# Kernel tuning notes

Measured on AMD Instinct MI355X. Metric: run time of the kernel, lower is better.

## Reference

```python
import jax, jax.numpy as jnp
import numpy as np

NEG = -1000000.0  # same finite mask value as the Triton kernel


def setup_inputs() -> dict:
    key = jax.random.key(0)
    k1, k2, k3, k4 = jax.random.split(key, 4)
    B, H, KVH, S, D = 1, 32, 8, 2048, 128
    return {
        "q": jax.random.normal(k1, (B, H, S, D), dtype=jnp.float32),
        "k": jax.random.normal(k2, (B, KVH, S, D), dtype=jnp.float32),
        "v": jax.random.normal(k3, (B, KVH, S, D), dtype=jnp.float32),
        "sinks": jax.random.normal(k4, (H,), dtype=jnp.float32),
        "bandwidth": 1024,
    }


def reference(q, k, v, sinks, bandwidth):
    """Prefill flash attention with causal + sliding-window masking, GQA, and
    per-head attention sinks (extra logit in the softmax denominator)."""
    B, H, S, D = q.shape
    ratio = H // k.shape[1]  # KV_HEAD_RATIO
    kf = jnp.repeat(k, ratio, axis=1)  # [B,H,S,D]
    vf = jnp.repeat(v, ratio, axis=1)
    sm_scale = 1.0 / np.sqrt(D).astype(np.float32)

    logits = jnp.einsum("bhqd,bhkd->bhqk", q, kf) * sm_scale  # [B,H,S,S]
    q_pos = jnp.arange(S)[:, None]
    k_pos = jnp.arange(S)[None, :]
    mask = k_pos > q_pos  # causal
    if bandwidth > 0:
        mask = mask | (k_pos < q_pos - bandwidth + 1)  # sliding window
    logits = jnp.where(mask, NEG, logits)

    sink = sinks[None, :, None]  # [1,H,1] broadcast over batch, query
    m = jnp.maximum(jnp.max(logits, axis=-1), sink)  # [B,H,S]
    p = jnp.exp(logits - m[..., None])
    denom = p.sum(axis=-1) + jnp.exp(sink - m)  # sink contributes to denom only
    out = jnp.einsum("bhqk,bhkd->bhqd", p, vf) / denom[..., None]
    return out
```

## Files before the change

kernel.cpp:

```cpp
#include <hip/hip_runtime.h>
#include <hip/hip_bf16.h>

typedef __bf16 bf16x8 __attribute__((ext_vector_type(8)));
typedef unsigned short u16x8 __attribute__((ext_vector_type(8)));
typedef unsigned int u32x4 __attribute__((ext_vector_type(4)));
typedef float f32x4 __attribute__((ext_vector_type(4)));

#define SLEN 2048
#define DDIM 128
#define NH   32
#define NKVH 8
#define KVB  32
#define MINIT  -1e30f
#define MASKED -3e30f
#define LOG2E  1.4426950408889634f

static __device__ __forceinline__ unsigned short f2bfu(float f) {
  union { float f; unsigned u; } x; x.f = f;
  return (unsigned short)((x.u + 0x7fffu + ((x.u >> 16) & 1u)) >> 16);
}
static __device__ __forceinline__ float bfu2f(unsigned short u) {
  union { unsigned u; float f; } x; x.u = ((unsigned)u) << 16;
  return x.f;
}
static __device__ __forceinline__ unsigned cvt_pk_bf16(float lo, float hi) {
  unsigned r;
  asm("v_cvt_pk_bf16_f32 %0, %1, %2" : "=v"(r) : "v"(lo), "v"(hi));
  return r;
}
static __device__ __forceinline__ f32x4 mfma_bf16(u16x8 a, u16x8 b, f32x4 c) {
  return __builtin_amdgcn_mfma_f32_16x16x32_bf16(
      __builtin_bit_cast(bf16x8, a), __builtin_bit_cast(bf16x8, b), c, 0, 0, 0);
}
static __device__ __forceinline__ int vswz_k(int row) {
  return (row & 3) | (((row >> 3) & 1) << 2);
}

__global__ __launch_bounds__(256) void conv_kv(const float* __restrict__ k,
                                               const float* __restrict__ v,
                                               unsigned* __restrict__ kdst,
                                               unsigned short* __restrict__ vt) {
  __shared__ unsigned T32[32][17];
  const int bb = blockIdx.x;
  if (bb < 1024) {
    const int i = bb * 256 + threadIdx.x;
    const float4 f0 = ((const float4*)k)[2 * i];
    const float4 f1 = ((const float4*)k)[2 * i + 1];
    u32x4 o = { cvt_pk_bf16(f0.x, f0.y), cvt_pk_bf16(f0.z, f0.w),
                cvt_pk_bf16(f1.x, f1.y), cvt_pk_bf16(f1.z, f1.w) };
    ((u32x4*)kdst)[i] = o;
    return;
  }
  const int b   = bb - 1024;
  const int dt  = b & 3;
  const int st  = (b >> 2) & 63;
  const int kvh = b >> 8;
  const int r  = threadIdx.x >> 3;
  const int cg = threadIdx.x & 7;
  const float4 f = *(const float4*)(v + ((size_t)(kvh * SLEN + st * 32 + r) * DDIM) + dt * 32 + cg * 4);
  T32[r][cg * 2]     = cvt_pk_bf16(f.x, f.y);
  T32[r][cg * 2 + 1] = cvt_pk_bf16(f.z, f.w);
  __syncthreads();
  const int dr = threadIdx.x >> 3;
  const unsigned sel = (dr & 1) ? 0x07060302u : 0x05040100u;
  const unsigned a0 = T32[cg * 4 + 0][dr >> 1], a1 = T32[cg * 4 + 1][dr >> 1];
  const unsigned a2 = T32[cg * 4 + 2][dr >> 1], a3 = T32[cg * 4 + 3][dr >> 1];
  unsigned short* vp = vt + (size_t)kvh * DDIM * SLEN + (size_t)(dt * 32 + dr) * SLEN + st * 32 + cg * 4;
  const unsigned w0 = __builtin_amdgcn_perm(a1, a0, sel);
  const unsigned w1 = __builtin_amdgcn_perm(a3, a2, sel);
  vp[0] = (unsigned short)(w0 & 0xffff);
  vp[1] = (unsigned short)(w0 >> 16);
  vp[2] = (unsigned short)(w1 & 0xffff);
  vp[3] = (unsigned short)(w1 >> 16);
}

template <int NCH>
__global__ __launch_bounds__(256, 4) void attn_fwd(
    const float* __restrict__ q, const unsigned short* __restrict__ kbf,
    const unsigned short* __restrict__ vtg, const float* __restrict__ sinks,
    const int* __restrict__ bwp, float* __restrict__ out,
    unsigned short* __restrict__ pO, float* __restrict__ pm,
    float* __restrict__ pl) {
  constexpr int NQT = 32;
  __shared__ unsigned short Kl[2][KVB * DDIM];
  __shared__ unsigned short Vt[2][DDIM * KVB];
  __shared__ float SmS[4][16];

  const int tid  = threadIdx.x;
  const int wid  = tid >> 6;
  const int lane = tid & 63;
  const int ln   = lane & 15;
  const int hi   = lane >> 4;

  const int B   = blockIdx.x;
  const int x   = B & 7;
  const int j   = B >> 3;
  constexpr int per = 4 * NCH;
  const int qt  = NQT - 1 - (j / per);
  const int rem = j % per;
  const int hh  = rem / NCH;
  const int c   = rem % NCH;
  const int h   = x * 4 + hh;
  const int kvh = x;
  const int q0  = qt * 64;
  const int qrow0 = q0 + wid * 16;
  const int qpos  = qrow0 + ln;

  const int bwv    = bwp[0];
  const int lo_off = (bwv > 0) ? (bwv - 1) : SLEN;

  const int T0 = max(0, q0 - lo_off) >> 5;
  const int T1 = (q0 + 63) >> 5;
  const int N  = T1 - T0 + 1;
  const int ch = (N + NCH - 1) / NCH;
  const int Ts = T0 + c * ch;
  const int Te = min(T1, Ts + ch - 1);

  const float c2 = 0.08838834764831845f * LOG2E;

  u16x8 qf[4];
  {
    const float* qp = q + ((size_t)(h * SLEN + qpos) * DDIM) + hi * 8;
    #pragma unroll
    for (int dk = 0; dk < 4; ++dk) {
      float4 f0 = *(const float4*)(qp + dk * 32);
      float4 f1 = *(const float4*)(qp + dk * 32 + 4);
      u32x4 t = { cvt_pk_bf16(f0.x, f0.y), cvt_pk_bf16(f0.z, f0.w),
                  cvt_pk_bf16(f1.x, f1.y), cvt_pk_bf16(f1.z, f1.w) };
      qf[dk] = __builtin_bit_cast(u16x8, t);
    }
  }

  float m2 = MINIT, l_ln = 0.0f;
  f32x4 oacc[8];
  #pragma unroll
  for (int nt = 0; nt < 8; ++nt) oacc[nt] = f32x4{0.f, 0.f, 0.f, 0.f};

  const unsigned short* Kg = kbf + (size_t)kvh * SLEN * DDIM;
  const unsigned short* Vg = vtg + (size_t)kvh * DDIM * SLEN;

  const int kr0 = tid >> 4, sk = tid & 15;
  const int kr1 = kr0 + 16;
  const int kw0 = kr0 * DDIM + (((sk & 8) | ((sk & 7) ^ vswz_k(kr0))) * 8);
  const int kw1 = kr1 * DDIM + (((sk & 8) | ((sk & 7) ^ vswz_k(kr1))) * 8);
  const int vr0 = tid >> 2, sv = tid & 3;
  const int vr1 = vr0 + 64;
  const int vw0 = vr0 * KVB + ((sv ^ ((vr0 >> 1) & 3)) * 8);
  const int vw1 = vr1 * KVB + ((sv ^ ((vr1 >> 1) & 3)) * 8);

  const int prow = ((ln >> 2) << 3) | (ln & 3);
  const int vk   = (ln & 3) | (((ln >> 2) & 1) << 2);
  int kfo[4];
  #pragma unroll
  for (int dk = 0; dk < 4; ++dk) {
    const int s = dk * 4 + hi;
    kfo[dk] = prow * DDIM + (((s & 8) | ((s & 7) ^ vk)) * 8);
  }
  const int vro = ln * KVB + ((hi ^ ((ln >> 1) & 3)) * 8);

  if (Ts <= Te) {
    const int kbS = Ts * 32, kbE = Te * 32;

    u16x8 pk0, pk1, pv0, pv1;
    pk0 = *(const u16x8*)(Kg + (size_t)(kbS + kr0) * DDIM + sk * 8);
    pk1 = *(const u16x8*)(Kg + (size_t)(kbS + kr1) * DDIM + sk * 8);
    pv0 = *(const u16x8*)(Vg + (size_t)vr0 * SLEN + kbS + sv * 8);
    pv1 = *(const u16x8*)(Vg + (size_t)vr1 * SLEN + kbS + sv * 8);
    *(u16x8*)&Kl[0][kw0] = pk0;
    *(u16x8*)&Kl[0][kw1] = pk1;
    *(u16x8*)&Vt[0][vw0] = pv0;
    *(u16x8*)&Vt[0][vw1] = pv1;
    {
      const int nb = min(kbS + KVB, kbE);
      pk0 = *(const u16x8*)(Kg + (size_t)(nb + kr0) * DDIM + sk * 8);
      pk1 = *(const u16x8*)(Kg + (size_t)(nb + kr1) * DDIM + sk * 8);
      pv0 = *(const u16x8*)(Vg + (size_t)vr0 * SLEN + nb + sv * 8);
      pv1 = *(const u16x8*)(Vg + (size_t)vr1 * SLEN + nb + sv * 8);
    }

    int cur = 0;
    for (int kb = kbS; kb <= kbE; kb += KVB) {
      __syncthreads();
      const int nxt = cur ^ 1;
      *(u16x8*)&Kl[nxt][kw0] = pk0;
      *(u16x8*)&Kl[nxt][kw1] = pk1;
      *(u16x8*)&Vt[nxt][vw0] = pv0;
      *(u16x8*)&Vt[nxt][vw1] = pv1;
      {
        const int nb = min(kb + 2 * KVB, kbE);
        pk0 = *(const u16x8*)(Kg + (size_t)(nb + kr0) * DDIM + sk * 8);
        pk1 = *(const u16x8*)(Kg + (size_t)(nb + kr1) * DDIM + sk * 8);
        pv0 = *(const u16x8*)(Vg + (size_t)vr0 * SLEN + nb + sv * 8);
        pv1 = *(const u16x8*)(Vg + (size_t)vr1 * SLEN + nb + sv * 8);
      }

      const bool skip = (kb > qrow0 + 15) || (kb + KVB - 1 < qrow0 - lo_off);
      if (!skip) {
        const unsigned short* kbp = &Kl[cur][0];
        const unsigned short* vbp = &Vt[cur][0];

        f32x4 sacc0 = {0,0,0,0}, sacc1 = {0,0,0,0};
        __builtin_amdgcn_s_setprio(1);
        #pragma unroll
        for (int dk = 0; dk < 4; ++dk) {
          sacc0 = mfma_bf16(*(const u16x8*)(kbp + kfo[dk]), qf[dk], sacc0);
          sacc1 = mfma_bf16(*(const u16x8*)(kbp + kfo[dk] + 4 * DDIM), qf[dk], sacc1);
        }
        __builtin_amdgcn_s_setprio(0);

        float p[8];
        const bool interior = (kb + KVB - 1 <= qrow0) && (kb >= qrow0 + 15 - lo_off);
        if (interior) {
          #pragma unroll
          for (int r = 0; r < 4; ++r) {
            p[r]     = sacc0[r] * c2;
            p[4 + r] = sacc1[r] * c2;
          }
        } else {
          #pragma unroll
          for (int r = 0; r < 4; ++r) {
            const int kp0 = kb + hi * 8 + r;
            const int kp1 = kp0 + 4;
            p[r]     = ((kp0 <= qpos) && (kp0 >= qpos - lo_off)) ? sacc0[r] * c2 : MASKED;
            p[4 + r] = ((kp1 <= qpos) && (kp1 >= qpos - lo_off)) ? sacc1[r] * c2 : MASKED;
          }
        }

        float mx = fmaxf(fmaxf(fmaxf(p[0], p[1]), fmaxf(p[2], p[3])),
                         fmaxf(fmaxf(p[4], p[5]), fmaxf(p[6], p[7])));
        mx = fmaxf(mx, __shfl_xor(mx, 16));
        mx = fmaxf(mx, __shfl_xor(mx, 32));

        if (__any(mx > m2 + 11.5415605f)) {
          const float mn   = fmaxf(m2, mx);
          const float corr = exp2f(m2 - mn);
          l_ln *= corr;
          m2 = mn;
          if (hi == 0) SmS[wid][ln] = corr;
          float c4[4];
          #pragma unroll
          for (int r = 0; r < 4; ++r) c4[r] = SmS[wid][hi * 4 + r];
          #pragma unroll
          for (int nt = 0; nt < 8; ++nt)
            #pragma unroll
            for (int r = 0; r < 4; ++r) oacc[nt][r] *= c4[r];
        }

        float s = 0.0f;
        #pragma unroll
        for (int jj = 0; jj < 8; ++jj) { p[jj] = exp2f(p[jj] - m2); s += p[jj]; }
        s += __shfl_xor(s, 16);
        s += __shfl_xor(s, 32);
        l_ln += s;

        const u32x4 paw = { cvt_pk_bf16(p[0], p[1]), cvt_pk_bf16(p[2], p[3]),
                            cvt_pk_bf16(p[4], p[5]), cvt_pk_bf16(p[6], p[7]) };
        const u16x8 pa = __builtin_bit_cast(u16x8, paw);

        __builtin_amdgcn_s_setprio(1);
        #pragma unroll
        for (int nt = 0; nt < 8; ++nt) {
          const u16x8 vb = *(const u16x8*)(vbp + vro + nt * 16 * KVB);
          oacc[nt] = mfma_bf16(pa, vb, oacc[nt]);
        }
        __builtin_amdgcn_s_setprio(0);
      }
      cur ^= 1;
    }
  }

  if (NCH == 1) {
    const float sk2 = sinks[h] * LOG2E;
    const float M  = fmaxf(m2, sk2);
    const float ed = exp2f(m2 - M);
    const float fac_ln = ed / (l_ln * ed + exp2f(sk2 - M));
    if (hi == 0) SmS[wid][ln] = fac_ln;
    float fac4[4];
    #pragma unroll
    for (int r = 0; r < 4; ++r) fac4[r] = SmS[wid][hi * 4 + r];
    #pragma unroll
    for (int r = 0; r < 4; ++r) {
      float* op = out + ((size_t)(h * SLEN + qrow0 + hi*4 + r) * DDIM) + ln;
      #pragma unroll
      for (int nt = 0; nt < 8; ++nt) op[nt * 16] = oacc[nt][r] * fac4[r];
    }
  } else {
    const size_t Lb = ((size_t)(h * NQT + qt)) * NCH + c;
    if (hi == 0) {
      pm[Lb * 64 + wid * 16 + ln] = m2;
      pl[Lb * 64 + wid * 16 + ln] = l_ln;
    }
    #pragma unroll
    for (int r = 0; r < 4; ++r) {
      unsigned short* po = pO + (Lb * 64 + wid * 16 + hi * 4 + r) * 128 + ln;
      #pragma unroll
      for (int nt = 0; nt < 8; ++nt) po[nt * 16] = f2bfu(oacc[nt][r]);
    }
  }
}

template <int NCH, int QBLK, int NQT>
__global__ __launch_bounds__(256) void mergeN(
    const unsigned short* __restrict__ pO, const float* __restrict__ pm,
    const float* __restrict__ pl, const float* __restrict__ sinks,
    float* __restrict__ out) {
  const int t    = blockIdx.x * 256 + threadIdx.x;
  const int rid  = t >> 2;
  const int d0   = (t & 3) * 32;
  const int h    = rid >> 11;
  const int qpos = rid & 2047;
  const int qt   = qpos / QBLK;
  const int lr   = qpos % QBLK;
  const size_t base = ((size_t)(h * NQT + qt) * NCH) * QBLK + lr;
  const float sk2 = sinks[h] * LOG2E;
  float mc[NCH], lc[NCH];
  float M = sk2;
  #pragma unroll
  for (int c = 0; c < NCH; ++c) {
    mc[c] = pm[base + (size_t)c * QBLK];
    lc[c] = pl[base + (size_t)c * QBLK];
    M = fmaxf(M, mc[c]);
  }
  float denom = exp2f(sk2 - M);
  float sc[NCH];
  #pragma unroll
  for (int c = 0; c < NCH; ++c) { sc[c] = exp2f(mc[c] - M); denom += lc[c] * sc[c]; }
  const float inv = 1.0f / denom;
  float o[32];
  #pragma unroll
  for (int i = 0; i < 32; ++i) o[i] = 0.f;
  #pragma unroll
  for (int c = 0; c < NCH; ++c) {
    const unsigned short* pp = pO + (base + (size_t)c * QBLK) * 128 + d0;
    const float s = sc[c] * inv;
    #pragma unroll
    for (int i = 0; i < 4; ++i) {
      u16x8 a = *(const u16x8*)(pp + i * 8);
      #pragma unroll
      for (int jj = 0; jj < 8; ++jj) o[i*8+jj] += bfu2f(a[jj]) * s;
    }
  }
  float* op = out + (size_t)rid * 128 + d0;
  #pragma unroll
  for (int i = 0; i < 8; ++i)
    *(float4*)(op + i*4) = make_float4(o[i*4], o[i*4+1], o[i*4+2], o[i*4+3]);
}

extern "C" void kernel_launch(void* const* d_in, const int* in_sizes, int n_in,
                              void* d_out, int out_size, void* d_ws, size_t ws_size,
                              hipStream_t stream) {
  const float* q     = (const float*)d_in[0];
  const float* k     = (const float*)d_in[1];
  const float* v     = (const float*)d_in[2];
  const float* sinks = (const float*)d_in[3];
  const int*   bw    = (const int*)d_in[4];
  float* out = (float*)d_out;

  const size_t kvElems = (size_t)NKVH * SLEN * DDIM;
  unsigned short* kbf = (unsigned short*)d_ws;
  unsigned short* vtg = kbf + kvElems;
  unsigned short* pO  = vtg + kvElems;

  const size_t nPart2 = (size_t)NH * 32 * 2 * 64;
  const size_t need2  = 4 * kvElems + nPart2 * 128 * 2 + nPart2 * 8;

  conv_kv<<<dim3(1024 + NKVH * 64 * 4), 256, 0, stream>>>(k, v, (unsigned*)kbf, vtg);

  if (ws_size >= need2) {
    float* pm = (float*)(pO + nPart2 * 128);
    float* pl = pm + nPart2;
    attn_fwd<2><<<dim3(2048), 256, 0, stream>>>(q, kbf, vtg, sinks, bw, out, pO, pm, pl);
    mergeN<2, 64, 32><<<dim3(1024), 256, 0, stream>>>(pO, pm, pl, sinks, out);
  } else {
    attn_fwd<1><<<dim3(1024), 256, 0, stream>>>(q, kbf, vtg, sinks, bw, out, pO, nullptr, nullptr);
  }
}
```

Baseline: 77.75 us.

## Single-buffer K/V LDS tiles, defer row-sum shuffles, remap merge blocks by KV head

Replaces the double-buffered K/V shared-memory tiles with a single buffer guarded by two barriers per iteration, and prefetches the next tile from global memory into registers only one step ahead. This halves LDS use, which may allow more resident blocks, but it serialises the LDS store with compute and adds a barrier. The per-iteration cross-lane reduction of the row sum is moved to a single reduction after the loop. The merge kernel's block-to-row mapping is changed to group heads by KV head.

```diff
diff --git a/kernel.cpp b/kernel.cpp
--- a/kernel.cpp
+++ b/kernel.cpp
@@ -82,8 +82,8 @@
     unsigned short* __restrict__ pO, float* __restrict__ pm,
     float* __restrict__ pl) {
   constexpr int NQT = 32;
-  __shared__ unsigned short Kl[2][KVB * DDIM];
-  __shared__ unsigned short Vt[2][DDIM * KVB];
+  __shared__ unsigned short Kl[KVB * DDIM];
+  __shared__ unsigned short Vt[DDIM * KVB];
   __shared__ float SmS[4][16];
 
   const int tid  = threadIdx.x;
@@ -131,7 +131,8 @@
     }
   }
 
-  float m2 = MINIT, l_ln = 0.0f;
+  float m2 = MINIT;
+  float l_ln = 0.0f;
   f32x4 oacc[8];
   #pragma unroll
   for (int nt = 0; nt < 8; ++nt) oacc[nt] = f32x4{0.f, 0.f, 0.f, 0.f};
@@ -162,112 +163,100 @@
     const int kbS = Ts * 32, kbE = Te * 32;
 
     u16x8 pk0, pk1, pv0, pv1;
-    pk0 = *(const u16x8*)(Kg + (size_t)(kbS + kr0) * DDIM + sk * 8);
-    pk1 = *(const u16x8*)(Kg + (size_t)(kbS + kr1) * DDIM + sk * 8);
-    pv0 = *(const u16x8*)(Vg + (size_t)vr0 * SLEN + kbS + sv * 8);
-    pv1 = *(const u16x8*)(Vg + (size_t)vr1 * SLEN + kbS + sv * 8);
-    *(u16x8*)&Kl[0][kw0] = pk0;
-    *(u16x8*)&Kl[0][kw1] = pk1;
-    *(u16x8*)&Vt[0][vw0] = pv0;
-    *(u16x8*)&Vt[0][vw1] = pv1;
     {
-      const int nb = min(kbS + KVB, kbE);
-      pk0 = *(const u16x8*)(Kg + (size_t)(nb + kr0) * DDIM + sk * 8);
-      pk1 = *(const u16x8*)(Kg + (size_t)(nb + kr1) * DDIM + sk * 8);
-      pv0 = *(const u16x8*)(Vg + (size_t)vr0 * SLEN + nb + sv * 8);
-      pv1 = *(const u16x8*)(Vg + (size_t)vr1 * SLEN + nb + sv * 8);
-    }
-
-    int cur = 0;
+      pk0 = *(const u16x8*)(Kg + (size_t)(kbS + kr0) * DDIM + sk * 8);
+      pk1 = *(const u16x8*)(Kg + (size_t)(kbS + kr1) * DDIM + sk * 8);
+      pv0 = *(const u16x8*)(Vg + (size_t)vr0 * SLEN + kbS + sv * 8);
+      pv1 = *(const u16x8*)(Vg + (size_t)vr1 * SLEN + kbS + sv * 8);
+    }
+
     for (int kb = kbS; kb <= kbE; kb += KVB) {
       __syncthreads();
-      const int nxt = cur ^ 1;
-      *(u16x8*)&Kl[nxt][kw0] = pk0;
-      *(u16x8*)&Kl[nxt][kw1] = pk1;
-      *(u16x8*)&Vt[nxt][vw0] = pv0;
-      *(u16x8*)&Vt[nxt][vw1] = pv1;
+      *(u16x8*)&Kl[kw0] = pk0;
+      *(u16x8*)&Kl[kw1] = pk1;
+      *(u16x8*)&Vt[vw0] = pv0;
+      *(u16x8*)&Vt[vw1] = pv1;
+      __syncthreads();
+
       {
-        const int nb = min(kb + 2 * KVB, kbE);
+        const int nb = min(kb + KVB, kbE);
         pk0 = *(const u16x8*)(Kg + (size_t)(nb + kr0) * DDIM + sk * 8);
         pk1 = *(const u16x8*)(Kg + (size_t)(nb + kr1) * DDIM + sk * 8);
         pv0 = *(const u16x8*)(Vg + (size_t)vr0 * SLEN + nb + sv * 8);
         pv1 = *(const u16x8*)(Vg + (size_t)vr1 * SLEN + nb + sv * 8);
       }
 
-      const bool skip = (kb > qrow0 + 15) || (kb + KVB - 1 < qrow0 - lo_off);
-      if (!skip) {
-        const unsigned short* kbp = &Kl[cur][0];
-        const unsigned short* vbp = &Vt[cur][0];
-
-        f32x4 sacc0 = {0,0,0,0}, sacc1 = {0,0,0,0};
-        __builtin_amdgcn_s_setprio(1);
+      if (kb > qrow0 + 15) continue;
+      if (kb + KVB - 1 < qrow0 - lo_off) continue;
+
+      f32x4 sacc0 = {0,0,0,0}, sacc1 = {0,0,0,0};
+      __builtin_amdgcn_s_setprio(1);
+      #pragma unroll
+      for (int dk = 0; dk < 4; ++dk) {
+        sacc0 = mfma_bf16(*(const u16x8*)&Kl[kfo[dk]], qf[dk], sacc0);
+        sacc1 = mfma_bf16(*(const u16x8*)&Kl[kfo[dk] + 4 * DDIM], qf[dk], sacc1);
+      }
+      __builtin_amdgcn_s_setprio(0);
+
+      float p[8];
+      const bool interior = (kb + KVB - 1 <= qrow0) && (kb >= qrow0 + 15 - lo_off);
+      if (interior) {
         #pragma unroll
-        for (int dk = 0; dk < 4; ++dk) {
-          sacc0 = mfma_bf16(*(const u16x8*)(kbp + kfo[dk]), qf[dk], sacc0);
-          sacc1 = mfma_bf16(*(const u16x8*)(kbp + kfo[dk] + 4 * DDIM), qf[dk], sacc1);
+        for (int r = 0; r < 4; ++r) {
+          p[r]     = sacc0[r] * c2;
+          p[4 + r] = sacc1[r] * c2;
         }
-        __builtin_amdgcn_s_setprio(0);
-
-        float p[8];
-        const bool interior = (kb + KVB - 1 <= qrow0) && (kb >= qrow0 + 15 - lo_off);
-        if (interior) {
+      } else {
+        #pragma unroll
+        for (int r = 0; r < 4; ++r) {
+          const int kp0 = kb + hi * 8 + r;
+          const int kp1 = kp0 + 4;
+          p[r]     = ((kp0 <= qpos) && (kp0 >= qpos - lo_off)) ? sacc0[r] * c2 : MASKED;
+          p[4 + r] = ((kp1 <= qpos) && (kp1 >= qpos - lo_off)) ? sacc1[r] * c2 : MASKED;
+        }
+      }
+
+      float mx = fmaxf(fmaxf(fmaxf(p[0], p[1]), fmaxf(p[2], p[3])),
+                       fmaxf(fmaxf(p[4], p[5]), fmaxf(p[6], p[7])));
+      mx = fmaxf(mx, __shfl_xor(mx, 16));
+      mx = fmaxf(mx, __shfl_xor(mx, 32));
+
+      if (__any(mx > m2 + 11.5415605f)) {
+        const float mn   = fmaxf(m2, mx);
+        const float corr = exp2f(m2 - mn);
+        l_ln *= corr;
+        m2 = mn;
+        if (hi == 0) SmS[wid][ln] = corr;
+        float c4[4];
+        #pragma unroll
+        for (int r = 0; r < 4; ++r) c4[r] = SmS[wid][hi * 4 + r];
+        #pragma unroll
+        for (int nt = 0; nt < 8; ++nt)
           #pragma unroll
-          for (int r = 0; r < 4; ++r) {
-            p[r]     = sacc0[r] * c2;
-            p[4 + r] = sacc1[r] * c2;
-          }
-        } else {
-          #pragma unroll
-          for (int r = 0; r < 4; ++r) {
-            const int kp0 = kb + hi * 8 + r;
-            const int kp1 = kp0 + 4;
-            p[r]     = ((kp0 <= qpos) && (kp0 >= qpos - lo_off)) ? sacc0[r] * c2 : MASKED;
-            p[4 + r] = ((kp1 <= qpos) && (kp1 >= qpos - lo_off)) ? sacc1[r] * c2 : MASKED;
-          }
-        }
-
-        float mx = fmaxf(fmaxf(fmaxf(p[0], p[1]), fmaxf(p[2], p[3])),
-                         fmaxf(fmaxf(p[4], p[5]), fmaxf(p[6], p[7])));
-        mx = fmaxf(mx, __shfl_xor(mx, 16));
-        mx = fmaxf(mx, __shfl_xor(mx, 32));
-
-        if (__any(mx > m2 + 11.5415605f)) {
-          const float mn   = fmaxf(m2, mx);
-          const float corr = exp2f(m2 - mn);
-          l_ln *= corr;
-          m2 = mn;
-          if (hi == 0) SmS[wid][ln] = corr;
-          float c4[4];
-          #pragma unroll
-          for (int r = 0; r < 4; ++r) c4[r] = SmS[wid][hi * 4 + r];
-          #pragma unroll
-          for (int nt = 0; nt < 8; ++nt)
-            #pragma unroll
-            for (int r = 0; r < 4; ++r) oacc[nt][r] *= c4[r];
-        }
-
-        float s = 0.0f;
-        #pragma unroll
-        for (int jj = 0; jj < 8; ++jj) { p[jj] = exp2f(p[jj] - m2); s += p[jj]; }
-        s += __shfl_xor(s, 16);
-        s += __shfl_xor(s, 32);
-        l_ln += s;
-
-        const u32x4 paw = { cvt_pk_bf16(p[0], p[1]), cvt_pk_bf16(p[2], p[3]),
-                            cvt_pk_bf16(p[4], p[5]), cvt_pk_bf16(p[6], p[7]) };
-        const u16x8 pa = __builtin_bit_cast(u16x8, paw);
-
-        __builtin_amdgcn_s_setprio(1);
-        #pragma unroll
-        for (int nt = 0; nt < 8; ++nt) {
-          const u16x8 vb = *(const u16x8*)(vbp + vro + nt * 16 * KVB);
-          oacc[nt] = mfma_bf16(pa, vb, oacc[nt]);
-        }
-        __builtin_amdgcn_s_setprio(0);
-      }
-      cur ^= 1;
-    }
-  }
+          for (int r = 0; r < 4; ++r) oacc[nt][r] *= c4[r];
+      }
+
+      float s = 0.0f;
+      #pragma unroll
+      for (int jj = 0; jj < 8; ++jj) { p[jj] = exp2f(p[jj] - m2); s += p[jj]; }
+      l_ln += s;
+
+      const u32x4 paw = { cvt_pk_bf16(p[0], p[1]), cvt_pk_bf16(p[2], p[3]),
+                          cvt_pk_bf16(p[4], p[5]), cvt_pk_bf16(p[6], p[7]) };
+      const u16x8 pa = __builtin_bit_cast(u16x8, paw);
+
+      __builtin_amdgcn_s_setprio(1);
+      #pragma unroll
+      for (int nt = 0; nt < 8; ++nt) {
+        const u16x8 vb = *(const u16x8*)&Vt[vro + nt * 16 * KVB];
+        oacc[nt] = mfma_bf16(pa, vb, oacc[nt]);
+      }
+      __builtin_amdgcn_s_setprio(0);
+    }
+  }
+
+  l_ln += __shfl_xor(l_ln, 16);
+  l_ln += __shfl_xor(l_ln, 32);
 
   if (NCH == 1) {
     const float sk2 = sinks[h] * LOG2E;
@@ -304,13 +293,16 @@
     const unsigned short* __restrict__ pO, const float* __restrict__ pm,
     const float* __restrict__ pl, const float* __restrict__ sinks,
     float* __restrict__ out) {
-  const int t    = blockIdx.x * 256 + threadIdx.x;
-  const int rid  = t >> 2;
-  const int d0   = (t & 3) * 32;
-  const int h    = rid >> 11;
-  const int qpos = rid & 2047;
-  const int qt   = qpos / QBLK;
-  const int lr   = qpos % QBLK;
+  const int b   = blockIdx.x;
+  const int x   = b & 7;
+  const int jj2 = b >> 3;
+  const int h   = x * 4 + (jj2 >> 5);
+  const int sub = jj2 & 31;
+  const int rloc = sub * 64 + (threadIdx.x >> 2);
+  const int rid  = h * 2048 + rloc;
+  const int d0   = (threadIdx.x & 3) * 32;
+  const int qt   = rloc / QBLK;
+  const int lr   = rloc % QBLK;
   const size_t base = ((size_t)(h * NQT + qt) * NCH) * QBLK + lr;
   const float sk2 = sinks[h] * LOG2E;
   float mc[NCH], lc[NCH];
```

Measured after the change: 75.37 us. -3.1%, faster.
